# Performance work log

Measured on AMD Instinct MI355X. Metric: run time of the kernel, lower is better.

The kernel has to match this reference:

```python
import jax, jax.numpy as jnp
import numpy as np

LN_EPS = 1e-5


def layer_norm(x, g, b):
    mu = jnp.mean(x, axis=-1, keepdims=True)
    var = jnp.mean(jnp.square(x - mu), axis=-1, keepdims=True)
    return (x - mu) * jax.lax.rsqrt(var + LN_EPS) * g + b


def setup_inputs() -> dict:
    key = jax.random.key(0)
    ks = jax.random.split(key, 8)
    N, E, D = 100000, 1000000, 128
    node_feat = jax.random.normal(ks[0], (N, D), dtype=jnp.float32)
    edge_index = jax.random.randint(ks[1], (2, E), 0, N, dtype=jnp.int64)
    s = 1.0 / np.sqrt(D)
    return {
        "node_feat": node_feat,
        "edge_index": edge_index,
        "layer_idx": 0,
        "ln1_g": jnp.ones((D,), jnp.float32),
        "ln1_b": jnp.zeros((D,), jnp.float32),
        "W_conv": jax.random.normal(ks[2], (D, D), jnp.float32) * s,
        "b_conv": jnp.zeros((D,), jnp.float32),
        "ln2_g": jnp.ones((D,), jnp.float32),
        "ln2_b": jnp.zeros((D,), jnp.float32),
        "W1": jax.random.normal(ks[3], (D, 4 * D), jnp.float32) * s,
        "b1": jnp.zeros((4 * D,), jnp.float32),
        "W2": jax.random.normal(ks[4], (4 * D, D), jnp.float32) * (0.5 * s),
        "b2": jnp.zeros((D,), jnp.float32),
    }


def reference(node_feat, edge_index, layer_idx, ln1_g, ln1_b, W_conv, b_conv,
              ln2_g, ln2_b, W1, b1, W2, b2):
    N = node_feat.shape[0]
    # DeepGCNLayer block='res+': x + conv(dropout(act(norm(x)))); dropout inert at eval
    h = jax.nn.gelu(layer_norm(node_feat, ln1_g, ln1_b), approximate=False)
    # GCNConv: symmetric-normalized aggregation with added self-loops
    hW = h @ W_conv                                         # [N, D]
    loops = jnp.arange(N, dtype=edge_index.dtype)
    src = jnp.concatenate([edge_index[0], loops])           # [E+N]
    dst = jnp.concatenate([edge_index[1], loops])
    deg = jax.ops.segment_sum(jnp.ones(src.shape, hW.dtype), dst, num_segments=N)
    dinv = jnp.where(deg > 0, jax.lax.rsqrt(deg), 0.0)
    coef = dinv[src] * dinv[dst]                            # [E+N]
    agg = jax.ops.segment_sum(hW[src] * coef[:, None], dst, num_segments=N)
    conv_feat = node_feat + agg + b_conv
    # FFN: LN -> Linear(D,4D) -> GELU -> Linear(4D,D) -> GELU, residual from node_feat
    f = layer_norm(conv_feat, ln2_g, ln2_b)
    f = jax.nn.gelu(f @ W1 + b1, approximate=False)
    f = jax.nn.gelu(f @ W2 + b2, approximate=False)
    return node_feat + f
```

## Files before the change

kernel.cpp:

```cpp
#include <hip/hip_runtime.h>
#include <math.h>


typedef _Float16 half8  __attribute__((ext_vector_type(8)));
typedef _Float16 half2v __attribute__((ext_vector_type(2)));
typedef __fp16   fp16x2 __attribute__((ext_vector_type(2)));
typedef float    floatx4 __attribute__((ext_vector_type(4)));

#define SBLK 128

__device__ __forceinline__ float gelu_f(float x){
  float x2 = x*x;
  float z  = x*(1.5957691216f + 0.07135481283f*x2);
  float e  = __expf(-z);
  return x * __builtin_amdgcn_rcpf(1.0f + e);
}
__device__ __forceinline__ unsigned pk16(float a, float b){
  fp16x2 h = __builtin_amdgcn_cvt_pkrtz(a, b);
  return __builtin_bit_cast(unsigned, h);
}
__device__ __forceinline__ float wave_reduce_sum(float v){
  #pragma unroll
  for (int off = 32; off > 0; off >>= 1) v += __shfl_xor(v, off, 64);
  return v;
}

__global__ __launch_bounds__(256) void k_hist(const int* __restrict__ ei, int* __restrict__ cnt,
                                              int E, int NB, int ESB){
  __shared__ int h[2048];
  int t = threadIdx.x;
  for (int i = t; i < NB; i += 256) h[i] = 0;
  __syncthreads();
  int e0 = blockIdx.x * ESB;
  int e1 = min(E, e0 + ESB);
  for (int e = e0 + t; e < e1; e += 256)
    atomicAdd(&h[ei[E + e] >> 6], 1);
  __syncthreads();
  for (int i = t; i < NB; i += 256) cnt[(size_t)blockIdx.x * NB + i] = h[i];
}

__global__ __launch_bounds__(128) void k_scanB(int* __restrict__ cnt, int* __restrict__ total,
                                               int NB){
  __shared__ int w0sum;
  int b = blockIdx.x;
  int t = threadIdx.x, l = t & 63, w = t >> 6;
  int v = cnt[(size_t)t*NB + b];
  int x = v;
  #pragma unroll
  for (int off = 1; off < 64; off <<= 1){
    int y = __shfl_up(x, off);
    if (l >= off) x += y;
  }
  if (w == 0 && l == 63) w0sum = x;
  __syncthreads();
  int ex = x - v + (w ? w0sum : 0);
  cnt[(size_t)t*NB + b] = ex;
  if (t == 127) total[b] = ex + v;
}

__global__ __launch_bounds__(256) void k_scan2(const int* __restrict__ total,
                                               int* __restrict__ bucketStart, int NB){
  __shared__ int wsum[4];
  int t = threadIdx.x, w = t >> 6, l = t & 63;
  int vals[8];
  int sum = 0;
  #pragma unroll
  for (int j = 0; j < 8; j++){
    int idx = t*8 + j;
    vals[j] = (idx < NB) ? total[idx] : 0;
    sum += vals[j];
  }
  int x = sum;
  #pragma unroll
  for (int off = 1; off < 64; off <<= 1){
    int y = __shfl_up(x, off);
    if (l >= off) x += y;
  }
  if (l == 63) wsum[w] = x;
  __syncthreads();
  if (t == 0){
    int s = 0;
    #pragma unroll
    for (int i = 0; i < 4; i++){ int c = wsum[i]; wsum[i] = s; s += c; }
  }
  __syncthreads();
  int run = wsum[w] + x - sum;
  #pragma unroll
  for (int j = 0; j < 8; j++){
    int idx = t*8 + j;
    if (idx < NB) bucketStart[idx] = run;
    run += vals[j];
  }
  if (t == 255) bucketStart[NB] = run;
}

__global__ __launch_bounds__(256) void k_scatter(const int* __restrict__ ei,
    const int* __restrict__ cnt, const int* __restrict__ bucketStart,
    int* __restrict__ eb, int E, int NB, int ESB){
  __shared__ int cur[2048];
  int t = threadIdx.x;
  for (int i = t; i < NB; i += 256)
    cur[i] = bucketStart[i] + cnt[(size_t)blockIdx.x*NB + i];
  __syncthreads();
  int e0 = blockIdx.x*ESB, e1 = min(E, e0 + ESB);
  for (int e = e0 + t; e < e1; e += 256){
    int s = ei[e], d = ei[E + e];
    int pos = atomicAdd(&cur[d >> 6], 1);
    eb[pos] = (s << 6) | (d & 63);
  }
}

__global__ __launch_bounds__(256) void k_sort2(const int* __restrict__ eb,
    const int* __restrict__ bucketStart, int* __restrict__ eSrc,
    int* __restrict__ row_start, int* __restrict__ incount,
    float* __restrict__ dinv, int N){
  __shared__ int hcnt[64];
  __shared__ int hcur[64];
  int b = blockIdx.x, t = threadIdx.x;
  if (t < 64) hcnt[t] = 0;
  __syncthreads();
  int s0 = bucketStart[b], s1 = bucketStart[b+1];
  for (int e = s0 + t; e < s1; e += 256) atomicAdd(&hcnt[eb[e] & 63], 1);
  __syncthreads();
  if (t < 64){
    int v = hcnt[t];
    int x = v;
    #pragma unroll
    for (int off = 1; off < 64; off <<= 1){
      int y = __shfl_up(x, off);
      if (t >= off) x += y;
    }
    int ex = x - v;
    hcur[t] = ex;
    int node = (b << 6) + t;
    if (node < N){
      row_start[node] = s0 + ex;
      incount[node]   = v;
      dinv[node]      = rsqrtf((float)v + 1.0f);
    }
  }
  __syncthreads();
  for (int e = s0 + t; e < s1; e += 256){
    int v = eb[e];
    int pos = atomicAdd(&hcur[v & 63], 1);
    eSrc[s0 + pos] = v >> 6;
  }
}

__global__ __launch_bounds__(256) void k_prep(
    const float* __restrict__ Wc, const float* __restrict__ W1, const float* __restrict__ W2,
    _Float16* __restrict__ Wcp, _Float16* __restrict__ W1p, _Float16* __restrict__ W2p,
    const float* __restrict__ nf, const float* __restrict__ g, const float* __restrict__ b,
    const float* __restrict__ dinv, _Float16* __restrict__ hs)
{
  int bid = blockIdx.x;
  if (bid < 72){
    int id = bid*256 + threadIdx.x;
    const float* W; _Float16* P; int K, Nc, base;
    if (id < 2048)            { W = Wc; P = Wcp; K = 128; Nc = 128; base = id; }
    else if (id < 2048+8192)  { W = W1; P = W1p; K = 128; Nc = 512; base = id - 2048; }
    else                      { W = W2; P = W2p; K = 512; Nc = 128; base = id - 10240; }
    int lane = base & 63;
    int nkb  = K >> 5;
    int kb   = (base >> 6) % nkb;
    int tile = base / (nkb << 6);
    int col  = (tile << 4) + (lane & 15);
    int k0   = (kb << 5) + ((lane >> 4) << 3);
    _Float16 v[8];
    #pragma unroll
    for (int j = 0; j < 8; j++) v[j] = (_Float16)W[(size_t)(k0 + j)*Nc + col];
    *(half8*)&P[(size_t)base * 8] = *(const half8*)v;
  } else {
    int w = threadIdx.x >> 6, l = threadIdx.x & 63;
    int node = (bid - 72)*4 + w;
    float2 x = *(const float2*)&nf[(size_t)node*128 + 2*l];
    float mu = wave_reduce_sum(x.x + x.y) * 0.0078125f;
    float d0 = x.x - mu, d1 = x.y - mu;
    float var = wave_reduce_sum(d0*d0 + d1*d1) * 0.0078125f;
    float rs = rsqrtf(var + 1e-5f);
    float dn = dinv[node];
    float y0 = dn * gelu_f(d0*rs*g[2*l]   + b[2*l]);
    float y1 = dn * gelu_f(d1*rs*g[2*l+1] + b[2*l+1]);
    *(unsigned*)&hs[(size_t)node*128 + 2*l] = pk16(y0, y1);
  }
}

__global__ __launch_bounds__(256) void k_gather(const _Float16* __restrict__ hs,
    const int* __restrict__ eSrc, const int* __restrict__ row_start,
    const int* __restrict__ incount, const float* __restrict__ dinv,
    _Float16* __restrict__ aggh, int N)
{
  int w = threadIdx.x >> 6, l = threadIdx.x & 63;
  int node = (blockIdx.x << 2) + w;
  int g  = l >> 3;
  int li = l & 7;
  float dn = dinv[node];
  int start = row_start[node], cnt = incount[node];
  float acc[16];
  #pragma unroll
  for (int i = 0; i < 16; i++) acc[i] = 0.f;
  for (int e = g; e < cnt + 1; e += 8){
    int s = (e == 0) ? node : eSrc[start + e - 1];
    const uint4* hp = (const uint4*)&hs[(size_t)s*128 + (li << 4)];
    uint4 v0 = hp[0], v1 = hp[1];
    half2v p0 = __builtin_bit_cast(half2v, v0.x), p1 = __builtin_bit_cast(half2v, v0.y);
    half2v p2 = __builtin_bit_cast(half2v, v0.z), p3 = __builtin_bit_cast(half2v, v0.w);
    half2v p4 = __builtin_bit_cast(half2v, v1.x), p5 = __builtin_bit_cast(half2v, v1.y);
    half2v p6 = __builtin_bit_cast(half2v, v1.z), p7 = __builtin_bit_cast(half2v, v1.w);
    acc[0]  += (float)p0.x; acc[1]  += (float)p0.y;
    acc[2]  += (float)p1.x; acc[3]  += (float)p1.y;
    acc[4]  += (float)p2.x; acc[5]  += (float)p2.y;
    acc[6]  += (float)p3.x; acc[7]  += (float)p3.y;
    acc[8]  += (float)p4.x; acc[9]  += (float)p4.y;
    acc[10] += (float)p5.x; acc[11] += (float)p5.y;
    acc[12] += (float)p6.x; acc[13] += (float)p6.y;
    acc[14] += (float)p7.x; acc[15] += (float)p7.y;
  }
  #pragma unroll
  for (int i = 0; i < 16; i++){
    acc[i] += __shfl_xor(acc[i], 8);
    acc[i] += __shfl_xor(acc[i], 16);
    acc[i] += __shfl_xor(acc[i], 32);
  }
  if (l < 8){
    uint4 o0, o1;
    o0.x = pk16(dn*acc[0],  dn*acc[1]);  o0.y = pk16(dn*acc[2],  dn*acc[3]);
    o0.z = pk16(dn*acc[4],  dn*acc[5]);  o0.w = pk16(dn*acc[6],  dn*acc[7]);
    o1.x = pk16(dn*acc[8],  dn*acc[9]);  o1.y = pk16(dn*acc[10], dn*acc[11]);
    o1.z = pk16(dn*acc[12], dn*acc[13]); o1.w = pk16(dn*acc[14], dn*acc[15]);
    uint4* op = (uint4*)&aggh[(size_t)node*128 + (l << 4)];
    op[0] = o0; op[1] = o1;
  }
}

__global__ __launch_bounds__(256) void k_ffn(
    const float* __restrict__ nf, const _Float16* __restrict__ aggh,
    const _Float16* __restrict__ Wcp, const float* __restrict__ bc,
    const float* __restrict__ g2, const float* __restrict__ bl2,
    const _Float16* __restrict__ W1p, const float* __restrict__ b1,
    const _Float16* __restrict__ W2p, const float* __restrict__ b2,
    float* __restrict__ out, int N)
{
  __shared__ __align__(16) unsigned short u_s[32*520];
  int t = threadIdx.x, w = t >> 6, l = t & 63;
  int nb = blockIdx.x << 5;
  int quad = l >> 4, ln16 = l & 15;

  {
    int m = t >> 3, c0 = (t & 7) << 4;
    const uint4* src = (const uint4*)&aggh[(size_t)(nb + m)*128 + c0];
    uint4 v0 = src[0], v1 = src[1];
    uint4* dst = (uint4*)&u_s[4352 + m*136 + c0];
    dst[0] = v0; dst[1] = v1;
  }
  __syncthreads();

  {
    half8 ag[2][4];
    #pragma unroll
    for (int mt = 0; mt < 2; mt++)
      #pragma unroll
      for (int kb = 0; kb < 4; kb++)
        ag[mt][kb] = *(const half8*)&u_s[4352 + ((mt << 4) + ln16)*136 + (kb << 5) + (quad << 3)];
    const half8* Wp8 = (const half8*)Wcp;
    #pragma unroll
    for (int nt = 0; nt < 2; nt++){
      int tile = (w << 1) + nt;
      half8 bf[4];
      #pragma unroll
      for (int kb = 0; kb < 4; kb++) bf[kb] = Wp8[(size_t)((tile << 2) + kb)*64 + l];
      floatx4 acc0 = {0.f,0.f,0.f,0.f}, acc1 = {0.f,0.f,0.f,0.f};
      #pragma unroll
      for (int kb = 0; kb < 4; kb++){
        acc0 = __builtin_amdgcn_mfma_f32_16x16x32_f16(ag[0][kb], bf[kb], acc0, 0, 0, 0);
        acc1 = __builtin_amdgcn_mfma_f32_16x16x32_f16(ag[1][kb], bf[kb], acc1, 0, 0, 0);
      }
      int col = (tile << 4) + ln16;
      float bcv = bc[col];
      #pragma unroll
      for (int r = 0; r < 4; r++){
        int m0 = (quad << 2) + r;
        *(_Float16*)&u_s[m0*136 + col]        = (_Float16)(acc0[r] + bcv);
        *(_Float16*)&u_s[(m0 + 16)*136 + col] = (_Float16)(acc1[r] + bcv);
      }
    }
  }
  __syncthreads();

  float2 nfr[8];
  #pragma unroll
  for (int q = 0; q < 8; q++){
    int m = (w << 3) + q;
    unsigned pu = *(unsigned*)&u_s[m*136 + 2*l];
    half2v hp = __builtin_bit_cast(half2v, pu);
    nfr[q] = *(const float2*)&nf[(size_t)(nb + m)*128 + 2*l];
    float x0 = (float)hp.x + nfr[q].x;
    float x1 = (float)hp.y + nfr[q].y;
    float mu = wave_reduce_sum(x0 + x1) * 0.0078125f;
    float d0 = x0 - mu, d1 = x1 - mu;
    float var = wave_reduce_sum(d0*d0 + d1*d1) * 0.0078125f;
    float rs = rsqrtf(var + 1e-5f);
    float y0 = d0*rs*g2[2*l]   + bl2[2*l];
    float y1 = d1*rs*g2[2*l+1] + bl2[2*l+1];
    *(unsigned*)&u_s[m*136 + 2*l] = pk16(y0, y1);
  }
  __syncthreads();

  half8 a[2][4];
  #pragma unroll
  for (int mt = 0; mt < 2; mt++)
    #pragma unroll
    for (int kb = 0; kb < 4; kb++)
      a[mt][kb] = *(const half8*)&u_s[((mt << 4) + ln16)*136 + (kb << 5) + (quad << 3)];
  __syncthreads();

  {
    const half8* Wp8 = (const half8*)W1p;
    #pragma unroll
    for (int nt = 0; nt < 8; nt++){
      int tile = (w << 3) + nt;
      half8 bf[4];
      #pragma unroll
      for (int kb = 0; kb < 4; kb++) bf[kb] = Wp8[(size_t)((tile << 2) + kb)*64 + l];
      floatx4 acc0 = {0.f,0.f,0.f,0.f}, acc1 = {0.f,0.f,0.f,0.f};
      #pragma unroll
      for (int kb = 0; kb < 4; kb++){
        acc0 = __builtin_amdgcn_mfma_f32_16x16x32_f16(a[0][kb], bf[kb], acc0, 0, 0, 0);
        acc1 = __builtin_amdgcn_mfma_f32_16x16x32_f16(a[1][kb], bf[kb], acc1, 0, 0, 0);
      }
      int col = (tile << 4) + ln16;
      float bv = b1[col];
      #pragma unroll
      for (int r = 0; r < 4; r++){
        *(_Float16*)&u_s[((quad << 2) + r)*520 + col]      = (_Float16)gelu_f(acc0[r] + bv);
        *(_Float16*)&u_s[(16 + (quad << 2) + r)*520 + col] = (_Float16)gelu_f(acc1[r] + bv);
      }
    }
  }
  __syncthreads();

  floatx4 acc00 = {0.f,0.f,0.f,0.f}, acc01 = {0.f,0.f,0.f,0.f};
  floatx4 acc10 = {0.f,0.f,0.f,0.f}, acc11 = {0.f,0.f,0.f,0.f};
  int tile0 = (w << 1), tile1 = tile0 + 1;
  {
    const half8* Wp8 = (const half8*)W2p;
    for (int kb = 0; kb < 16; kb++){
      half8 a0 = *(const half8*)&u_s[ln16*520        + (kb << 5) + (quad << 3)];
      half8 a1 = *(const half8*)&u_s[(16 + ln16)*520 + (kb << 5) + (quad << 3)];
      half8 b0  = Wp8[(size_t)((tile0 << 4) + kb)*64 + l];
      half8 b1v = Wp8[(size_t)((tile1 << 4) + kb)*64 + l];
      acc00 = __builtin_amdgcn_mfma_f32_16x16x32_f16(a0, b0,  acc00, 0, 0, 0);
      acc01 = __builtin_amdgcn_mfma_f32_16x16x32_f16(a0, b1v, acc01, 0, 0, 0);
      acc10 = __builtin_amdgcn_mfma_f32_16x16x32_f16(a1, b0,  acc10, 0, 0, 0);
      acc11 = __builtin_amdgcn_mfma_f32_16x16x32_f16(a1, b1v, acc11, 0, 0, 0);
    }
  }
  __syncthreads();

  {
    float* fs = (float*)u_s;
    int col0 = (tile0 << 4) + ln16, col1 = (tile1 << 4) + ln16;
    float bv0 = b2[col0], bv1 = b2[col1];
    #pragma unroll
    for (int r = 0; r < 4; r++){
      int m0 = (quad << 2) + r;
      fs[m0*132 + col0]        = gelu_f(acc00[r] + bv0);
      fs[m0*132 + col1]        = gelu_f(acc01[r] + bv1);
      fs[(m0 + 16)*132 + col0] = gelu_f(acc10[r] + bv0);
      fs[(m0 + 16)*132 + col1] = gelu_f(acc11[r] + bv1);
    }
  }
  __syncthreads();

  {
    const float* fs = (const float*)u_s;
    #pragma unroll
    for (int q = 0; q < 8; q++){
      int m = (w << 3) + q;
      float2 o;
      o.x = nfr[q].x + fs[m*132 + 2*l];
      o.y = nfr[q].y + fs[m*132 + 2*l + 1];
      *(float2*)&out[(size_t)(nb + m)*128 + 2*l] = o;
    }
  }
}

extern "C" void kernel_launch(void* const* d_in, const int* in_sizes, int n_in,
                              void* d_out, int out_size, void* d_ws, size_t ws_size,
                              hipStream_t stream) {
  const float* nf   = (const float*)d_in[0];
  const int*   ei   = (const int*)  d_in[1];
  const float* ln1g = (const float*)d_in[3];
  const float* ln1b = (const float*)d_in[4];
  const float* Wc   = (const float*)d_in[5];
  const float* bc   = (const float*)d_in[6];
  const float* ln2g = (const float*)d_in[7];
  const float* ln2b = (const float*)d_in[8];
  const float* W1   = (const float*)d_in[9];
  const float* b1   = (const float*)d_in[10];
  const float* W2   = (const float*)d_in[11];
  const float* b2   = (const float*)d_in[12];
  float* out = (float*)d_out;

  int N = in_sizes[0] / 128;
  int E = in_sizes[1] / 2;
  int NB  = (N + 63) >> 6;
  int ESB = (E + SBLK - 1) / SBLK;

  char* ws = (char*)d_ws;
  _Float16* hs   = (_Float16*)ws;
  _Float16* aggh = (_Float16*)(ws + (size_t)N*128*2);
  char* p = ws + (size_t)N*128*4;
  p = (char*)(((size_t)p + 15) & ~(size_t)15);
  int*   cnt         = (int*)p;   p += (size_t)SBLK*NB*4;
  int*   total       = (int*)p;   p += (size_t)NB*4;
  int*   bucketStart = (int*)p;   p += (size_t)(NB+1)*4;
  float* dinv        = (float*)p; p += (size_t)N*4;
  int*   incount     = (int*)p;   p += (size_t)N*4;
  int*   row_start   = (int*)p;   p += (size_t)N*4;
  int*   eb          = (int*)p;   p += (size_t)E*4;
  int*   eSrc        = (int*)p;   p += (size_t)E*4;
  p = (char*)(((size_t)p + 15) & ~(size_t)15);
  _Float16* Wcp = (_Float16*)p; p += (size_t)2048*8*2;
  _Float16* W1p = (_Float16*)p; p += (size_t)8192*8*2;
  _Float16* W2p = (_Float16*)p; p += (size_t)8192*8*2;

  k_hist   <<<SBLK, 256, 0, stream>>>(ei, cnt, E, NB, ESB);
  k_scanB  <<<NB, 128, 0, stream>>>(cnt, total, NB);
  k_scan2  <<<1, 256, 0, stream>>>(total, bucketStart, NB);
  k_scatter<<<SBLK, 256, 0, stream>>>(ei, cnt, bucketStart, eb, E, NB, ESB);
  k_sort2  <<<NB, 256, 0, stream>>>(eb, bucketStart, eSrc, row_start, incount, dinv, N);

  k_prep   <<<72 + N/4, 256, 0, stream>>>(Wc, W1, W2, Wcp, W1p, W2p, nf, ln1g, ln1b, dinv, hs);
  k_gather <<<N/4, 256, 0, stream>>>(hs, eSrc, row_start, incount, dinv, aggh, N);
  k_ffn    <<<N/32, 256, 0, stream>>>(nf, aggh, Wcp, bc, ln2g, ln2b, W1p, b1, W2p, b2, out, N);
}
```

Before: 287.1 us.

## Shrink FFN kernel LDS and registers by chunking hidden dimension for occupancy

Restructures the fused FFN kernel so the 512-wide hidden activation is processed in two 256-column chunks for each 16-row half. This cuts shared memory from about 33KB to 17KB and drops the register-held A fragments and nf values. Launch bounds request 8 blocks per CU to raise occupancy. In exchange, the W1 and W2 weights are reloaded per half, there are more syncthreads, and the output is written as scattered scalar stores with nf re-read from global memory.

Measured after the change: 885.2 us. 3.08x slower.

```diff
diff --git a/kernel.cpp b/kernel.cpp
--- a/kernel.cpp
+++ b/kernel.cpp
@@ -233,7 +233,7 @@
   }
 }
 
-__global__ __launch_bounds__(256) void k_ffn(
+__global__ __launch_bounds__(256, 8) void k_ffn(
     const float* __restrict__ nf, const _Float16* __restrict__ aggh,
     const _Float16* __restrict__ Wcp, const float* __restrict__ bc,
     const float* __restrict__ g2, const float* __restrict__ bl2,
@@ -241,7 +241,7 @@
     const _Float16* __restrict__ W2p, const float* __restrict__ b2,
     float* __restrict__ out, int N)
 {
-  __shared__ __align__(16) unsigned short u_s[32*520];
+  __shared__ __align__(16) unsigned short u_s[8704];
   int t = threadIdx.x, w = t >> 6, l = t & 63;
   int nb = blockIdx.x << 5;
   int quad = l >> 4, ln16 = l & 15;
@@ -256,12 +256,6 @@
   __syncthreads();
 
   {
-    half8 ag[2][4];
-    #pragma unroll
-    for (int mt = 0; mt < 2; mt++)
-      #pragma unroll
-      for (int kb = 0; kb < 4; kb++)
-        ag[mt][kb] = *(const half8*)&u_s[4352 + ((mt << 4) + ln16)*136 + (kb << 5) + (quad << 3)];
     const half8* Wp8 = (const half8*)Wcp;
     #pragma unroll
     for (int nt = 0; nt < 2; nt++){
@@ -269,118 +263,93 @@
       half8 bf[4];
       #pragma unroll
       for (int kb = 0; kb < 4; kb++) bf[kb] = Wp8[(size_t)((tile << 2) + kb)*64 + l];
-      floatx4 acc0 = {0.f,0.f,0.f,0.f}, acc1 = {0.f,0.f,0.f,0.f};
-      #pragma unroll
-      for (int kb = 0; kb < 4; kb++){
-        acc0 = __builtin_amdgcn_mfma_f32_16x16x32_f16(ag[0][kb], bf[kb], acc0, 0, 0, 0);
-        acc1 = __builtin_amdgcn_mfma_f32_16x16x32_f16(ag[1][kb], bf[kb], acc1, 0, 0, 0);
-      }
       int col = (tile << 4) + ln16;
       float bcv = bc[col];
       #pragma unroll
-      for (int r = 0; r < 4; r++){
-        int m0 = (quad << 2) + r;
-        *(_Float16*)&u_s[m0*136 + col]        = (_Float16)(acc0[r] + bcv);
-        *(_Float16*)&u_s[(m0 + 16)*136 + col] = (_Float16)(acc1[r] + bcv);
+      for (int mt = 0; mt < 2; mt++){
+        floatx4 acc = {0.f,0.f,0.f,0.f};
+        #pragma unroll
+        for (int kb = 0; kb < 4; kb++){
+          half8 ag = *(const half8*)&u_s[4352 + ((mt << 4) + ln16)*136 + (kb << 5) + (quad << 3)];
+          acc = __builtin_amdgcn_mfma_f32_16x16x32_f16(ag, bf[kb], acc, 0, 0, 0);
+        }
+        #pragma unroll
+        for (int r = 0; r < 4; r++)
+          *(_Float16*)&u_s[((mt << 4) + (quad << 2) + r)*136 + col] = (_Float16)(acc[r] + bcv);
       }
     }
   }
   __syncthreads();
 
-  float2 nfr[8];
-  #pragma unroll
-  for (int q = 0; q < 8; q++){
-    int m = (w << 3) + q;
-    unsigned pu = *(unsigned*)&u_s[m*136 + 2*l];
-    half2v hp = __builtin_bit_cast(half2v, pu);
-    nfr[q] = *(const float2*)&nf[(size_t)(nb + m)*128 + 2*l];
-    float x0 = (float)hp.x + nfr[q].x;
-    float x1 = (float)hp.y + nfr[q].y;
-    float mu = wave_reduce_sum(x0 + x1) * 0.0078125f;
-    float d0 = x0 - mu, d1 = x1 - mu;
-    float var = wave_reduce_sum(d0*d0 + d1*d1) * 0.0078125f;
-    float rs = rsqrtf(var + 1e-5f);
-    float y0 = d0*rs*g2[2*l]   + bl2[2*l];
-    float y1 = d1*rs*g2[2*l+1] + bl2[2*l+1];
-    *(unsigned*)&u_s[m*136 + 2*l] = pk16(y0, y1);
-  }
-  __syncthreads();
-
-  half8 a[2][4];
-  #pragma unroll
-  for (int mt = 0; mt < 2; mt++)
-    #pragma unroll
-    for (int kb = 0; kb < 4; kb++)
-      a[mt][kb] = *(const half8*)&u_s[((mt << 4) + ln16)*136 + (kb << 5) + (quad << 3)];
-  __syncthreads();
-
   {
-    const half8* Wp8 = (const half8*)W1p;
-    #pragma unroll
-    for (int nt = 0; nt < 8; nt++){
-      int tile = (w << 3) + nt;
-      half8 bf[4];
-      #pragma unroll
-      for (int kb = 0; kb < 4; kb++) bf[kb] = Wp8[(size_t)((tile << 2) + kb)*64 + l];
-      floatx4 acc0 = {0.f,0.f,0.f,0.f}, acc1 = {0.f,0.f,0.f,0.f};
-      #pragma unroll
-      for (int kb = 0; kb < 4; kb++){
-        acc0 = __builtin_amdgcn_mfma_f32_16x16x32_f16(a[0][kb], bf[kb], acc0, 0, 0, 0);
-        acc1 = __builtin_amdgcn_mfma_f32_16x16x32_f16(a[1][kb], bf[kb], acc1, 0, 0, 0);
-      }
-      int col = (tile << 4) + ln16;
-      float bv = b1[col];
-      #pragma unroll
-      for (int r = 0; r < 4; r++){
-        *(_Float16*)&u_s[((quad << 2) + r)*520 + col]      = (_Float16)gelu_f(acc0[r] + bv);
-        *(_Float16*)&u_s[(16 + (quad << 2) + r)*520 + col] = (_Float16)gelu_f(acc1[r] + bv);
-      }
-    }
-  }
-  __syncthreads();
-
-  floatx4 acc00 = {0.f,0.f,0.f,0.f}, acc01 = {0.f,0.f,0.f,0.f};
-  floatx4 acc10 = {0.f,0.f,0.f,0.f}, acc11 = {0.f,0.f,0.f,0.f};
-  int tile0 = (w << 1), tile1 = tile0 + 1;
-  {
-    const half8* Wp8 = (const half8*)W2p;
-    for (int kb = 0; kb < 16; kb++){
-      half8 a0 = *(const half8*)&u_s[ln16*520        + (kb << 5) + (quad << 3)];
-      half8 a1 = *(const half8*)&u_s[(16 + ln16)*520 + (kb << 5) + (quad << 3)];
-      half8 b0  = Wp8[(size_t)((tile0 << 4) + kb)*64 + l];
-      half8 b1v = Wp8[(size_t)((tile1 << 4) + kb)*64 + l];
-      acc00 = __builtin_amdgcn_mfma_f32_16x16x32_f16(a0, b0,  acc00, 0, 0, 0);
-      acc01 = __builtin_amdgcn_mfma_f32_16x16x32_f16(a0, b1v, acc01, 0, 0, 0);
-      acc10 = __builtin_amdgcn_mfma_f32_16x16x32_f16(a1, b0,  acc10, 0, 0, 0);
-      acc11 = __builtin_amdgcn_mfma_f32_16x16x32_f16(a1, b1v, acc11, 0, 0, 0);
-    }
-  }
-  __syncthreads();
-
-  {
-    float* fs = (float*)u_s;
-    int col0 = (tile0 << 4) + ln16, col1 = (tile1 << 4) + ln16;
-    float bv0 = b2[col0], bv1 = b2[col1];
-    #pragma unroll
-    for (int r = 0; r < 4; r++){
-      int m0 = (quad << 2) + r;
-      fs[m0*132 + col0]        = gelu_f(acc00[r] + bv0);
-      fs[m0*132 + col1]        = gelu_f(acc01[r] + bv1);
-      fs[(m0 + 16)*132 + col0] = gelu_f(acc10[r] + bv0);
-      fs[(m0 + 16)*132 + col1] = gelu_f(acc11[r] + bv1);
-    }
-  }
-  __syncthreads();
-
-  {
-    const float* fs = (const float*)u_s;
+    float ga = g2[2*l], gb = g2[2*l+1], ba = bl2[2*l], bb = bl2[2*l+1];
     #pragma unroll
     for (int q = 0; q < 8; q++){
       int m = (w << 3) + q;
-      float2 o;
-      o.x = nfr[q].x + fs[m*132 + 2*l];
-      o.y = nfr[q].y + fs[m*132 + 2*l + 1];
-      *(float2*)&out[(size_t)(nb + m)*128 + 2*l] = o;
+      unsigned pu = *(unsigned*)&u_s[m*136 + 2*l];
+      half2v hp = __builtin_bit_cast(half2v, pu);
+      float2 nv = *(const float2*)&nf[(size_t)(nb + m)*128 + 2*l];
+      float x0 = (float)hp.x + nv.x;
+      float x1 = (float)hp.y + nv.y;
+      float mu = wave_reduce_sum(x0 + x1) * 0.0078125f;
+      float d0 = x0 - mu, d1 = x1 - mu;
+      float var = wave_reduce_sum(d0*d0 + d1*d1) * 0.0078125f;
+      float rs = rsqrtf(var + 1e-5f);
+      float y0 = d0*rs*ga + ba;
+      float y1 = d1*rs*gb + bb;
+      *(unsigned*)&u_s[m*136 + 2*l] = pk16(y0, y1);
+    }
+  }
+  __syncthreads();
+
+  const half8* W1p8 = (const half8*)W1p;
+  const half8* W2p8 = (const half8*)W2p;
+  int tile0 = (w << 1), tile1 = tile0 + 1;
+  int col0 = (tile0 << 4) + ln16, col1 = (tile1 << 4) + ln16;
+  float bv20 = b2[col0], bv21 = b2[col1];
+
+  for (int h = 0; h < 2; h++){
+    half8 ah[4];
+    #pragma unroll
+    for (int kb = 0; kb < 4; kb++)
+      ah[kb] = *(const half8*)&u_s[((h << 4) + ln16)*136 + (kb << 5) + (quad << 3)];
+    floatx4 acc0 = {0.f,0.f,0.f,0.f}, acc1 = {0.f,0.f,0.f,0.f};
+    for (int p = 0; p < 2; p++){
+      #pragma unroll
+      for (int nt = 0; nt < 4; nt++){
+        int tile = (p << 4) + (w << 2) + nt;
+        half8 bf[4];
+        #pragma unroll
+        for (int kb = 0; kb < 4; kb++) bf[kb] = W1p8[(size_t)((tile << 2) + kb)*64 + l];
+        floatx4 acc = {0.f,0.f,0.f,0.f};
+        #pragma unroll
+        for (int kb = 0; kb < 4; kb++)
+          acc = __builtin_amdgcn_mfma_f32_16x16x32_f16(ah[kb], bf[kb], acc, 0, 0, 0);
+        int colg = (tile << 4) + ln16;
+        int lcol = colg - (p << 8);
+        float bv = b1[colg];
+        #pragma unroll
+        for (int r = 0; r < 4; r++)
+          *(_Float16*)&u_s[4352 + ((quad << 2) + r)*264 + lcol] = (_Float16)gelu_f(acc[r] + bv);
+      }
+      __syncthreads();
+      #pragma unroll
+      for (int kbl = 0; kbl < 8; kbl++){
+        half8 a0 = *(const half8*)&u_s[4352 + ln16*264 + (kbl << 5) + (quad << 3)];
+        int kbg = (p << 3) + kbl;
+        half8 b0  = W2p8[(size_t)((tile0 << 4) + kbg)*64 + l];
+        half8 b1v = W2p8[(size_t)((tile1 << 4) + kbg)*64 + l];
+        acc0 = __builtin_amdgcn_mfma_f32_16x16x32_f16(a0, b0,  acc0, 0, 0, 0);
+        acc1 = __builtin_amdgcn_mfma_f32_16x16x32_f16(a0, b1v, acc1, 0, 0, 0);
+      }
+      __syncthreads();
+    }
+    #pragma unroll
+    for (int r = 0; r < 4; r++){
+      int m = (h << 4) + (quad << 2) + r;
+      size_t base = (size_t)(nb + m)*128;
+      out[base + col0] = nf[base + col0] + gelu_f(acc0[r] + bv20);
+      out[base + col1] = nf[base + col1] + gelu_f(acc1[r] + bv21);
     }
   }
 }
```

## Fuse histogram with LN1/GELU prep and move source-degree scaling into gather

Applied to the files above, without the earlier changes.

The per-node LN1+GELU prep and the weight repacking now run in the same launch as the edge-destination histogram, so they no longer have to wait for the degree computation. To remove that dependency, the source-side dinv factor is no longer folded into hs. The gather now loads dinv[s] per edge and applies it with an FMA. This removes one kernel launch and serialization point, in exchange for an extra random 4-byte load per edge in the gather.

Result: no change. 286.8 us (-0.1%).

```diff
diff --git a/kernel.cpp b/kernel.cpp
--- a/kernel.cpp
+++ b/kernel.cpp
@@ -26,136 +26,26 @@
 }
 
 __global__ __launch_bounds__(256) void k_hist(const int* __restrict__ ei, int* __restrict__ cnt,
-                                              int E, int NB, int ESB){
-  __shared__ int h[2048];
-  int t = threadIdx.x;
-  for (int i = t; i < NB; i += 256) h[i] = 0;
-  __syncthreads();
-  int e0 = blockIdx.x * ESB;
-  int e1 = min(E, e0 + ESB);
-  for (int e = e0 + t; e < e1; e += 256)
-    atomicAdd(&h[ei[E + e] >> 6], 1);
-  __syncthreads();
-  for (int i = t; i < NB; i += 256) cnt[(size_t)blockIdx.x * NB + i] = h[i];
-}
-
-__global__ __launch_bounds__(128) void k_scanB(int* __restrict__ cnt, int* __restrict__ total,
-                                               int NB){
-  __shared__ int w0sum;
-  int b = blockIdx.x;
-  int t = threadIdx.x, l = t & 63, w = t >> 6;
-  int v = cnt[(size_t)t*NB + b];
-  int x = v;
-  #pragma unroll
-  for (int off = 1; off < 64; off <<= 1){
-    int y = __shfl_up(x, off);
-    if (l >= off) x += y;
-  }
-  if (w == 0 && l == 63) w0sum = x;
-  __syncthreads();
-  int ex = x - v + (w ? w0sum : 0);
-  cnt[(size_t)t*NB + b] = ex;
-  if (t == 127) total[b] = ex + v;
-}
-
-__global__ __launch_bounds__(256) void k_scan2(const int* __restrict__ total,
-                                               int* __restrict__ bucketStart, int NB){
-  __shared__ int wsum[4];
-  int t = threadIdx.x, w = t >> 6, l = t & 63;
-  int vals[8];
-  int sum = 0;
-  #pragma unroll
-  for (int j = 0; j < 8; j++){
-    int idx = t*8 + j;
-    vals[j] = (idx < NB) ? total[idx] : 0;
-    sum += vals[j];
-  }
-  int x = sum;
-  #pragma unroll
-  for (int off = 1; off < 64; off <<= 1){
-    int y = __shfl_up(x, off);
-    if (l >= off) x += y;
-  }
-  if (l == 63) wsum[w] = x;
-  __syncthreads();
-  if (t == 0){
-    int s = 0;
-    #pragma unroll
-    for (int i = 0; i < 4; i++){ int c = wsum[i]; wsum[i] = s; s += c; }
-  }
-  __syncthreads();
-  int run = wsum[w] + x - sum;
-  #pragma unroll
-  for (int j = 0; j < 8; j++){
-    int idx = t*8 + j;
-    if (idx < NB) bucketStart[idx] = run;
-    run += vals[j];
-  }
-  if (t == 255) bucketStart[NB] = run;
-}
-
-__global__ __launch_bounds__(256) void k_scatter(const int* __restrict__ ei,
-    const int* __restrict__ cnt, const int* __restrict__ bucketStart,
-    int* __restrict__ eb, int E, int NB, int ESB){
-  __shared__ int cur[2048];
-  int t = threadIdx.x;
-  for (int i = t; i < NB; i += 256)
-    cur[i] = bucketStart[i] + cnt[(size_t)blockIdx.x*NB + i];
-  __syncthreads();
-  int e0 = blockIdx.x*ESB, e1 = min(E, e0 + ESB);
-  for (int e = e0 + t; e < e1; e += 256){
-    int s = ei[e], d = ei[E + e];
-    int pos = atomicAdd(&cur[d >> 6], 1);
-    eb[pos] = (s << 6) | (d & 63);
-  }
-}
-
-__global__ __launch_bounds__(256) void k_sort2(const int* __restrict__ eb,
-    const int* __restrict__ bucketStart, int* __restrict__ eSrc,
-    int* __restrict__ row_start, int* __restrict__ incount,
-    float* __restrict__ dinv, int N){
-  __shared__ int hcnt[64];
-  __shared__ int hcur[64];
-  int b = blockIdx.x, t = threadIdx.x;
-  if (t < 64) hcnt[t] = 0;
-  __syncthreads();
-  int s0 = bucketStart[b], s1 = bucketStart[b+1];
-  for (int e = s0 + t; e < s1; e += 256) atomicAdd(&hcnt[eb[e] & 63], 1);
-  __syncthreads();
-  if (t < 64){
-    int v = hcnt[t];
-    int x = v;
-    #pragma unroll
-    for (int off = 1; off < 64; off <<= 1){
-      int y = __shfl_up(x, off);
-      if (t >= off) x += y;
-    }
-    int ex = x - v;
-    hcur[t] = ex;
-    int node = (b << 6) + t;
-    if (node < N){
-      row_start[node] = s0 + ex;
-      incount[node]   = v;
-      dinv[node]      = rsqrtf((float)v + 1.0f);
-    }
-  }
-  __syncthreads();
-  for (int e = s0 + t; e < s1; e += 256){
-    int v = eb[e];
-    int pos = atomicAdd(&hcur[v & 63], 1);
-    eSrc[s0 + pos] = v >> 6;
-  }
-}
-
-__global__ __launch_bounds__(256) void k_prep(
+                                              int E, int NB, int ESB,
     const float* __restrict__ Wc, const float* __restrict__ W1, const float* __restrict__ W2,
     _Float16* __restrict__ Wcp, _Float16* __restrict__ W1p, _Float16* __restrict__ W2p,
     const float* __restrict__ nf, const float* __restrict__ g, const float* __restrict__ b,
-    const float* __restrict__ dinv, _Float16* __restrict__ hs)
+    _Float16* __restrict__ hs)
 {
   int bid = blockIdx.x;
-  if (bid < 72){
-    int id = bid*256 + threadIdx.x;
+  if (bid < SBLK){
+    __shared__ int h[2048];
+    int t = threadIdx.x;
+    for (int i = t; i < NB; i += 256) h[i] = 0;
+    __syncthreads();
+    int e0 = bid * ESB;
+    int e1 = min(E, e0 + ESB);
+    for (int e = e0 + t; e < e1; e += 256)
+      atomicAdd(&h[ei[E + e] >> 6], 1);
+    __syncthreads();
+    for (int i = t; i < NB; i += 256) cnt[(size_t)bid * NB + i] = h[i];
+  } else if (bid < SBLK + 72){
+    int id = (bid - SBLK)*256 + threadIdx.x;
     const float* W; _Float16* P; int K, Nc, base;
     if (id < 2048)            { W = Wc; P = Wcp; K = 128; Nc = 128; base = id; }
     else if (id < 2048+8192)  { W = W1; P = W1p; K = 128; Nc = 512; base = id - 2048; }
@@ -172,16 +62,123 @@
     *(half8*)&P[(size_t)base * 8] = *(const half8*)v;
   } else {
     int w = threadIdx.x >> 6, l = threadIdx.x & 63;
-    int node = (bid - 72)*4 + w;
+    int node = (bid - SBLK - 72)*4 + w;
     float2 x = *(const float2*)&nf[(size_t)node*128 + 2*l];
     float mu = wave_reduce_sum(x.x + x.y) * 0.0078125f;
     float d0 = x.x - mu, d1 = x.y - mu;
     float var = wave_reduce_sum(d0*d0 + d1*d1) * 0.0078125f;
     float rs = rsqrtf(var + 1e-5f);
-    float dn = dinv[node];
-    float y0 = dn * gelu_f(d0*rs*g[2*l]   + b[2*l]);
-    float y1 = dn * gelu_f(d1*rs*g[2*l+1] + b[2*l+1]);
+    float y0 = gelu_f(d0*rs*g[2*l]   + b[2*l]);
+    float y1 = gelu_f(d1*rs*g[2*l+1] + b[2*l+1]);
     *(unsigned*)&hs[(size_t)node*128 + 2*l] = pk16(y0, y1);
+  }
+}
+
+__global__ __launch_bounds__(128) void k_scanB(int* __restrict__ cnt, int* __restrict__ total,
+                                               int NB){
+  __shared__ int w0sum;
+  int b = blockIdx.x;
+  int t = threadIdx.x, l = t & 63, w = t >> 6;
+  int v = cnt[(size_t)t*NB + b];
+  int x = v;
+  #pragma unroll
+  for (int off = 1; off < 64; off <<= 1){
+    int y = __shfl_up(x, off);
+    if (l >= off) x += y;
+  }
+  if (w == 0 && l == 63) w0sum = x;
+  __syncthreads();
+  int ex = x - v + (w ? w0sum : 0);
+  cnt[(size_t)t*NB + b] = ex;
+  if (t == 127) total[b] = ex + v;
+}
+
+__global__ __launch_bounds__(256) void k_scan2(const int* __restrict__ total,
+                                               int* __restrict__ bucketStart, int NB){
+  __shared__ int wsum[4];
+  int t = threadIdx.x, w = t >> 6, l = t & 63;
+  int vals[8];
+  int sum = 0;
+  #pragma unroll
+  for (int j = 0; j < 8; j++){
+    int idx = t*8 + j;
+    vals[j] = (idx < NB) ? total[idx] : 0;
+    sum += vals[j];
+  }
+  int x = sum;
+  #pragma unroll
+  for (int off = 1; off < 64; off <<= 1){
+    int y = __shfl_up(x, off);
+    if (l >= off) x += y;
+  }
+  if (l == 63) wsum[w] = x;
+  __syncthreads();
+  if (t == 0){
+    int s = 0;
+    #pragma unroll
+    for (int i = 0; i < 4; i++){ int c = wsum[i]; wsum[i] = s; s += c; }
+  }
+  __syncthreads();
+  int run = wsum[w] + x - sum;
+  #pragma unroll
+  for (int j = 0; j < 8; j++){
+    int idx = t*8 + j;
+    if (idx < NB) bucketStart[idx] = run;
+    run += vals[j];
+  }
+  if (t == 255) bucketStart[NB] = run;
+}
+
+__global__ __launch_bounds__(256) void k_scatter(const int* __restrict__ ei,
+    const int* __restrict__ cnt, const int* __restrict__ bucketStart,
+    int* __restrict__ eb, int E, int NB, int ESB){
+  __shared__ int cur[2048];
+  int t = threadIdx.x;
+  for (int i = t; i < NB; i += 256)
+    cur[i] = bucketStart[i] + cnt[(size_t)blockIdx.x*NB + i];
+  __syncthreads();
+  int e0 = blockIdx.x*ESB, e1 = min(E, e0 + ESB);
+  for (int e = e0 + t; e < e1; e += 256){
+    int s = ei[e], d = ei[E + e];
+    int pos = atomicAdd(&cur[d >> 6], 1);
+    eb[pos] = (s << 6) | (d & 63);
+  }
+}
+
+__global__ __launch_bounds__(256) void k_sort2(const int* __restrict__ eb,
+    const int* __restrict__ bucketStart, int* __restrict__ eSrc,
+    int* __restrict__ row_start, int* __restrict__ incount,
+    float* __restrict__ dinv, int N){
+  __shared__ int hcnt[64];
+  __shared__ int hcur[64];
+  int b = blockIdx.x, t = threadIdx.x;
+  if (t < 64) hcnt[t] = 0;
+  __syncthreads();
+  int s0 = bucketStart[b], s1 = bucketStart[b+1];
+  for (int e = s0 + t; e < s1; e += 256) atomicAdd(&hcnt[eb[e] & 63], 1);
+  __syncthreads();
+  if (t < 64){
+    int v = hcnt[t];
+    int x = v;
+    #pragma unroll
+    for (int off = 1; off < 64; off <<= 1){
+      int y = __shfl_up(x, off);
+      if (t >= off) x += y;
+    }
+    int ex = x - v;
+    hcur[t] = ex;
+    int node = (b << 6) + t;
+    if (node < N){
+      row_start[node] = s0 + ex;
+      incount[node]   = v;
+      dinv[node]      = rsqrtf((float)v + 1.0f);
+    }
+  }
+  __syncthreads();
+  for (int e = s0 + t; e < s1; e += 256){
+    int v = eb[e];
+    int pos = atomicAdd(&hcur[v & 63], 1);
+    eSrc[s0 + pos] = v >> 6;
   }
 }
 
@@ -201,20 +198,21 @@
   for (int i = 0; i < 16; i++) acc[i] = 0.f;
   for (int e = g; e < cnt + 1; e += 8){
     int s = (e == 0) ? node : eSrc[start + e - 1];
+    float ds = dinv[s];
     const uint4* hp = (const uint4*)&hs[(size_t)s*128 + (li << 4)];
     uint4 v0 = hp[0], v1 = hp[1];
     half2v p0 = __builtin_bit_cast(half2v, v0.x), p1 = __builtin_bit_cast(half2v, v0.y);
     half2v p2 = __builtin_bit_cast(half2v, v0.z), p3 = __builtin_bit_cast(half2v, v0.w);
     half2v p4 = __builtin_bit_cast(half2v, v1.x), p5 = __builtin_bit_cast(half2v, v1.y);
     half2v p6 = __builtin_bit_cast(half2v, v1.z), p7 = __builtin_bit_cast(half2v, v1.w);
-    acc[0]  += (float)p0.x; acc[1]  += (float)p0.y;
-    acc[2]  += (float)p1.x; acc[3]  += (float)p1.y;
-    acc[4]  += (float)p2.x; acc[5]  += (float)p2.y;
-    acc[6]  += (float)p3.x; acc[7]  += (float)p3.y;
-    acc[8]  += (float)p4.x; acc[9]  += (float)p4.y;
-    acc[10] += (float)p5.x; acc[11] += (float)p5.y;
-    acc[12] += (float)p6.x; acc[13] += (float)p6.y;
-    acc[14] += (float)p7.x; acc[15] += (float)p7.y;
+    acc[0]  = fmaf((float)p0.x, ds, acc[0]);  acc[1]  = fmaf((float)p0.y, ds, acc[1]);
+    acc[2]  = fmaf((float)p1.x, ds, acc[2]);  acc[3]  = fmaf((float)p1.y, ds, acc[3]);
+    acc[4]  = fmaf((float)p2.x, ds, acc[4]);  acc[5]  = fmaf((float)p2.y, ds, acc[5]);
+    acc[6]  = fmaf((float)p3.x, ds, acc[6]);  acc[7]  = fmaf((float)p3.y, ds, acc[7]);
+    acc[8]  = fmaf((float)p4.x, ds, acc[8]);  acc[9]  = fmaf((float)p4.y, ds, acc[9]);
+    acc[10] = fmaf((float)p5.x, ds, acc[10]); acc[11] = fmaf((float)p5.y, ds, acc[11]);
+    acc[12] = fmaf((float)p6.x, ds, acc[12]); acc[13] = fmaf((float)p6.y, ds, acc[13]);
+    acc[14] = fmaf((float)p7.x, ds, acc[14]); acc[15] = fmaf((float)p7.y, ds, acc[15]);
   }
   #pragma unroll
   for (int i = 0; i < 16; i++){
@@ -425,13 +423,14 @@
   _Float16* W1p = (_Float16*)p; p += (size_t)8192*8*2;
   _Float16* W2p = (_Float16*)p; p += (size_t)8192*8*2;
 
-  k_hist   <<<SBLK, 256, 0, stream>>>(ei, cnt, E, NB, ESB);
+  k_hist   <<<SBLK + 72 + N/4, 256, 0, stream>>>(ei, cnt, E, NB, ESB,
+                                                 Wc, W1, W2, Wcp, W1p, W2p,
+                                                 nf, ln1g, ln1b, hs);
   k_scanB  <<<NB, 128, 0, stream>>>(cnt, total, NB);
   k_scan2  <<<1, 256, 0, stream>>>(total, bucketStart, NB);
   k_scatter<<<SBLK, 256, 0, stream>>>(ei, cnt, bucketStart, eb, E, NB, ESB);
   k_sort2  <<<NB, 256, 0, stream>>>(eb, bucketStart, eSrc, row_start, incount, dinv, N);
 
-  k_prep   <<<72 + N/4, 256, 0, stream>>>(Wc, W1, W2, Wcp, W1p, W2p, nf, ln1g, ln1b, dinv, hs);
   k_gather <<<N/4, 256, 0, stream>>>(hs, eSrc, row_start, incount, dinv, aggh, N);
   k_ffn    <<<N/32, 256, 0, stream>>>(nf, aggh, Wcp, bc, ln2g, ln2b, W1p, b1, W2p, b2, out, N);
 }
```
